# Optimization experiments

Hardware: AMD Instinct MI355X
Metric: run time of the kernel (lower is better)

Reference implementation:

```python
import jax, jax.numpy as jnp
import numpy as np

B, L, D, H, MLP = 8, 1024, 768, 12, 3072
DH = D // H
EPS = 1e-5


def setup_inputs() -> dict:
    key = jax.random.key(0)
    ks = jax.random.split(key, 8)
    s = 0.02
    return {
        "x": jax.random.normal(ks[0], (B, L, D), dtype=jnp.float32),
        "ln1_g": jnp.ones((D,), jnp.float32),
        "ln1_b": jnp.zeros((D,), jnp.float32),
        "w_qkv": jax.random.normal(ks[1], (3 * D, D), dtype=jnp.float32) * s,
        "w_out": jax.random.normal(ks[2], (D, D), dtype=jnp.float32) * s,
        "b_out": jnp.zeros((D,), jnp.float32),
        "ln2_g": jnp.ones((D,), jnp.float32),
        "ln2_b": jnp.zeros((D,), jnp.float32),
        "w1": jax.random.normal(ks[3], (MLP, D), dtype=jnp.float32) * s,
        "b1": jnp.zeros((MLP,), jnp.float32),
        "w2": jax.random.normal(ks[4], (D, MLP), dtype=jnp.float32) * s,
        "b2": jnp.zeros((D,), jnp.float32),
    }


def _layernorm(x, g, b):
    mu = jnp.mean(x, axis=-1, keepdims=True)
    var = jnp.mean(jnp.square(x - mu), axis=-1, keepdims=True)
    return (x - mu) * jax.lax.rsqrt(var + EPS) * g + b


def reference(x, ln1_g, ln1_b, w_qkv, w_out, b_out, ln2_g, ln2_b, w1, b1, w2, b2):
    # --- self-attention branch ---
    xn = _layernorm(x, ln1_g, ln1_b)                     # [B, L, D]
    qkv = jnp.einsum('bld,ed->ble', xn, w_qkv)           # [B, L, 3D]
    # rearrange 'b l (qkv h d) -> qkv b h l d'
    qkv = qkv.reshape(B, L, 3, H, DH).transpose(2, 0, 3, 1, 4)
    q, k, v = qkv[0], qkv[1], qkv[2]                     # [B, H, L, DH]
    scale = DH ** -0.5
    att = jnp.einsum('bhxd,bhyd->bhxy', q, k) * scale    # [B, H, L, L]
    att = jax.nn.softmax(att, axis=-1)
    o = jnp.einsum('bhxy,bhyd->bhxd', att, v)            # [B, H, L, DH]
    o = o.transpose(0, 2, 1, 3).reshape(B, L, D)         # 'b h l d -> b l (h d)'
    o = jnp.einsum('bld,ed->ble', o, w_out) + b_out
    x = x + o
    # --- MLP branch ---
    xn = _layernorm(x, ln2_g, ln2_b)
    h = jax.nn.gelu(jnp.einsum('bld,md->blm', xn, w1) + b1, approximate=False)
    h = jnp.einsum('blm,dm->bld', h, w2) + b2
    return x + h
```

## Files before the change

### kernel.cpp

```cpp
#include <hip/hip_runtime.h>
#include <hip/hip_bf16.h>
#include <math.h>

#define NB 8
#define NL 1024
#define ND 768
#define NH 12
#define NDH 64
#define NMLP 3072
#define NROWS 8192

typedef __attribute__((ext_vector_type(8))) short short8;
typedef __attribute__((ext_vector_type(8))) __bf16 bf16x8;
typedef __attribute__((ext_vector_type(4))) float f32x4;
typedef __attribute__((ext_vector_type(4))) float float4v;
typedef __attribute__((ext_vector_type(4))) unsigned short ushort4v;

__device__ __forceinline__ unsigned short f2b(float f) {
  unsigned u = __float_as_uint(f);
  unsigned r = (u + 0x7fffu + ((u >> 16) & 1u)) >> 16;
  return (unsigned short)r;
}

__device__ __forceinline__ f32x4 mfma16(short8 a, short8 b, f32x4 c) {
  return __builtin_amdgcn_mfma_f32_16x16x32_bf16(
      __builtin_bit_cast(bf16x8, a), __builtin_bit_cast(bf16x8, b), c, 0, 0, 0);
}

__device__ __forceinline__ void gl_lds16(const void* g, void* l) {
  __builtin_amdgcn_global_load_lds(
      (__attribute__((address_space(1))) void*)g,
      (__attribute__((address_space(3))) void*)l, 16, 0, 0);
}

__global__ __launch_bounds__(256) void cvt_all(const float* __restrict__ s0,
                                               const float* __restrict__ s1,
                                               const float* __restrict__ s2,
                                               const float* __restrict__ s3,
                                               unsigned short* __restrict__ d) {
  int i = (blockIdx.x * 256 + threadIdx.x) * 4;
  const float* s;
  int off;
  if (i < 1769472) { s = s0; off = i; }
  else if (i < 2359296) { s = s1; off = i - 1769472; }
  else if (i < 4718592) { s = s2; off = i - 2359296; }
  else { s = s3; off = i - 4718592; }
  float4v v = *(const float4v*)(s + off);
  ushort4v o;
  o[0] = f2b(v[0]); o[1] = f2b(v[1]); o[2] = f2b(v[2]); o[3] = f2b(v[3]);
  *(ushort4v*)(d + i) = o;
}

__global__ __launch_bounds__(256) void ln_bf16(const float* __restrict__ x,
                                               const float* __restrict__ g,
                                               const float* __restrict__ b,
                                               unsigned short* __restrict__ out) {
  int row = blockIdx.x, tid = threadIdx.x;
  const float* xr = x + (size_t)row * ND;
  float v0 = xr[tid], v1 = xr[tid + 256], v2 = xr[tid + 512];
  float s = v0 + v1 + v2;
  __shared__ float red[8];
#pragma unroll
  for (int o = 32; o > 0; o >>= 1) s += __shfl_down(s, o);
  int wv = tid >> 6, ln = tid & 63;
  if (ln == 0) red[wv] = s;
  __syncthreads();
  float mu = (red[0] + red[1] + red[2] + red[3]) * (1.0f / 768.0f);
  float d0 = v0 - mu, d1 = v1 - mu, d2 = v2 - mu;
  float q = d0 * d0 + d1 * d1 + d2 * d2;
#pragma unroll
  for (int o = 32; o > 0; o >>= 1) q += __shfl_down(q, o);
  if (ln == 0) red[4 + wv] = q;
  __syncthreads();
  float var = (red[4] + red[5] + red[6] + red[7]) * (1.0f / 768.0f);
  float rs = rsqrtf(var + 1e-5f);
  unsigned short* orow = out + (size_t)row * ND;
  orow[tid]       = f2b(d0 * rs * g[tid]       + b[tid]);
  orow[tid + 256] = f2b(d1 * rs * g[tid + 256] + b[tid + 256]);
  orow[tid + 512] = f2b(d2 * rs * g[tid + 512] + b[tid + 512]);
}

template <int MODE>
__global__ __launch_bounds__(512) void gemm128(
    const unsigned short* __restrict__ A, const unsigned short* __restrict__ W,
    unsigned short* __restrict__ outB, float* __restrict__ outF,
    const float* __restrict__ bias, const float* __restrict__ resid,
    int M, int N, int K, int gx) {
  __shared__ __attribute__((aligned(16))) unsigned short As[2 * 8192];
  __shared__ __attribute__((aligned(16))) unsigned short Bs[2 * 8192];

  const int nwg = gridDim.x;
  const int bid = blockIdx.x;
  const int q = nwg >> 3, r = nwg & 7;
  const int xcd = bid & 7, idx = bid >> 3;
  const int swz = (xcd < r ? xcd * (q + 1) : r * (q + 1) + (xcd - r) * q) + idx;
  const int by = swz / gx, bx = swz - by * gx;
  const int m0 = by * 128, n0 = bx * 128;

  const int tid = threadIdx.x;
  const int wave = tid >> 6, lane = tid & 63;
  const int l15 = lane & 15, lhi = lane >> 4;
  const int sw = l15 & 7;
  const int wm = wave >> 2, wn = wave & 3;

  const int sr = tid >> 3;
  const int swc8 = ((tid & 7) ^ (sr & 7)) * 8;
  const unsigned short* Aga = A + (size_t)(m0 + sr) * K + swc8;
  const unsigned short* Wga = W + (size_t)(n0 + sr) * K + swc8;

  f32x4 acc[4][2];
#pragma unroll
  for (int i = 0; i < 4; i++)
#pragma unroll
    for (int j = 0; j < 2; j++) acc[i][j] = (f32x4){0.f, 0.f, 0.f, 0.f};

  auto STAGE = [&](int kelem, int buf) {
    unsigned short* Ad = As + buf * 8192 + wave * 512;
    unsigned short* Bd = Bs + buf * 8192 + wave * 512;
    gl_lds16(Aga + kelem, Ad);
    gl_lds16(Aga + (size_t)64 * K + kelem, Ad + 4096);
    gl_lds16(Wga + kelem, Bd);
    gl_lds16(Wga + (size_t)64 * K + kelem, Bd + 4096);
  };

  const int NT = K >> 6;
  STAGE(0, 0);

  for (int t = 0; t < NT; ++t) {
    const int cb = t & 1;
    asm volatile("s_waitcnt vmcnt(0)" ::: "memory");
    __builtin_amdgcn_s_barrier();

    const unsigned short* Ac = As + cb * 8192;
    const unsigned short* Bc = Bs + cb * 8192;
    short8 af[4][2], bf[2][2];
#pragma unroll
    for (int i = 0; i < 4; i++) {
      int ar = wm * 64 + i * 16 + l15;
#pragma unroll
      for (int kk = 0; kk < 2; kk++)
        af[i][kk] = *(const short8*)&Ac[ar * 64 + (((kk * 4 + lhi) ^ sw) * 8)];
    }
#pragma unroll
    for (int j = 0; j < 2; j++) {
      int br = wn * 32 + j * 16 + l15;
#pragma unroll
      for (int kk = 0; kk < 2; kk++)
        bf[j][kk] = *(const short8*)&Bc[br * 64 + (((kk * 4 + lhi) ^ sw) * 8)];
    }
    if (t + 1 < NT) STAGE((t + 1) * 64, cb ^ 1);
#pragma unroll
    for (int kk = 0; kk < 2; kk++)
#pragma unroll
      for (int i = 0; i < 4; i++)
#pragma unroll
        for (int j = 0; j < 2; j++)
          acc[i][j] = mfma16(af[i][kk], bf[j][kk], acc[i][j]);
  }

#pragma unroll
  for (int i = 0; i < 4; i++) {
    int row = m0 + wm * 64 + i * 16 + lhi * 4;
#pragma unroll
    for (int j = 0; j < 2; j++) {
      int col = n0 + wn * 32 + j * 16 + l15;
#pragma unroll
      for (int r2 = 0; r2 < 4; r2++) {
        float v = acc[i][j][r2];
        size_t idxo = (size_t)(row + r2) * N + col;
        if (MODE == 0) {
          outB[idxo] = f2b(v);
        } else if (MODE == 2) {
          float t2 = v + bias[col];
          float z = 1.5957691f * t2 * (1.0f + 0.044715f * t2 * t2);
          float e = __expf(-z);
          outB[idxo] = f2b(__fdividef(t2, 1.0f + e));
        } else {
          outF[idxo] = v + bias[col] + resid[idxo];
        }
      }
    }
  }
}

template <int MODE>
__global__ __launch_bounds__(256) void gemm64(
    const unsigned short* __restrict__ A, const unsigned short* __restrict__ W,
    float* __restrict__ outF, const float* __restrict__ bias,
    const float* __restrict__ resid, int M, int N, int K, int gx) {
  __shared__ __attribute__((aligned(16))) unsigned short As[2 * 4096];
  __shared__ __attribute__((aligned(16))) unsigned short Bs[2 * 8192];

  const int nwg = gridDim.x;
  const int bid = blockIdx.x;
  const int q = nwg >> 3, r = nwg & 7;
  const int xcd = bid & 7, idx = bid >> 3;
  const int swz = (xcd < r ? xcd * (q + 1) : r * (q + 1) + (xcd - r) * q) + idx;
  const int by = swz / gx, bx = swz - by * gx;
  const int m0 = by * 64, n0 = bx * 128;

  const int tid = threadIdx.x;
  const int wave = tid >> 6, lane = tid & 63;
  const int l15 = lane & 15, lhi = lane >> 4;
  const int wn = wave;

  const int sr = tid >> 3;
  const int swc8 = ((tid & 7) ^ (sr & 7)) * 8;
  const unsigned short* Aga = A + (size_t)(m0 + sr) * K + swc8;
  const unsigned short* Wga = W + (size_t)(n0 + sr) * K + swc8;

  f32x4 acc[4][2];
#pragma unroll
  for (int i = 0; i < 4; i++)
#pragma unroll
    for (int j = 0; j < 2; j++) acc[i][j] = (f32x4){0.f, 0.f, 0.f, 0.f};

  auto STAGE = [&](int kelem, int buf) {
    unsigned short* Ad = As + buf * 4096 + wave * 512;
    unsigned short* Bd = Bs + buf * 8192 + wave * 512;
    gl_lds16(Aga + kelem, Ad);
    gl_lds16(Aga + (size_t)32 * K + kelem, Ad + 2048);
    gl_lds16(Wga + kelem, Bd);
    gl_lds16(Wga + (size_t)32 * K + kelem, Bd + 2048);
    gl_lds16(Wga + (size_t)64 * K + kelem, Bd + 4096);
    gl_lds16(Wga + (size_t)96 * K + kelem, Bd + 6144);
  };

  const int NT = K >> 6;
  STAGE(0, 0);

  for (int t = 0; t < NT; ++t) {
    const int cb = t & 1;
    if (t + 1 < NT) {
      STAGE((t + 1) * 64, cb ^ 1);
      asm volatile("s_waitcnt vmcnt(6)" ::: "memory");
    } else {
      asm volatile("s_waitcnt vmcnt(0)" ::: "memory");
    }
    __builtin_amdgcn_s_barrier();

    const unsigned short* Ac = As + cb * 4096;
    const unsigned short* Bc = Bs + cb * 8192;
    short8 af[4][2], bf[2][2];
#pragma unroll
    for (int i = 0; i < 4; i++) {
      int ar = i * 16 + l15;
#pragma unroll
      for (int kk = 0; kk < 2; kk++)
        af[i][kk] = *(const short8*)&Ac[ar * 64 + (((kk * 4 + lhi) ^ (ar & 7)) * 8)];
    }
#pragma unroll
    for (int j = 0; j < 2; j++) {
      int br = wn * 32 + j * 16 + l15;
#pragma unroll
      for (int kk = 0; kk < 2; kk++)
        bf[j][kk] = *(const short8*)&Bc[br * 64 + (((kk * 4 + lhi) ^ (br & 7)) * 8)];
    }
#pragma unroll
    for (int kk = 0; kk < 2; kk++)
#pragma unroll
      for (int i = 0; i < 4; i++)
#pragma unroll
        for (int j = 0; j < 2; j++)
          acc[i][j] = mfma16(af[i][kk], bf[j][kk], acc[i][j]);

    asm volatile("s_waitcnt lgkmcnt(0)" ::: "memory");
    __builtin_amdgcn_s_barrier();
  }

#pragma unroll
  for (int i = 0; i < 4; i++) {
    int row = m0 + i * 16 + lhi * 4;
#pragma unroll
    for (int j = 0; j < 2; j++) {
      int col = n0 + wn * 32 + j * 16 + l15;
#pragma unroll
      for (int r2 = 0; r2 < 4; r2++) {
        size_t idxo = (size_t)(row + r2) * N + col;
        outF[idxo] = acc[i][j][r2] + bias[col] + resid[idxo];
      }
    }
  }
}

__global__ __launch_bounds__(256) void vtrans(const unsigned short* __restrict__ qkv,
                                              unsigned short* __restrict__ vT) {
  int bid = blockIdx.x;
  int tt = bid & 15;
  int t2 = bid >> 4;
  int h = t2 % NH, b = t2 / NH;
  __shared__ unsigned short L[64 * 72];
  int t = threadIdx.x;
  int row0 = t >> 3;
  int col8 = (t & 7) * 8;
#pragma unroll
  for (int s = 0; s < 2; s++) {
    int row = row0 + s * 32;
    const unsigned short* src =
        qkv + ((size_t)(b * NL + tt * 64 + row)) * 2304 + 1536 + h * 64 + col8;
    short8 v = *(const short8*)src;
    int wchunk = row >> 3;
#pragma unroll
    for (int j = 0; j < 8; j++) {
      int d = col8 + j;
      int cp = wchunk ^ (d >> 3);
      L[d * 72 + cp * 8 + (row & 7)] = (unsigned short)v[j];
    }
  }
  __syncthreads();
#pragma unroll
  for (int s = 0; s < 2; s++) {
    int d = (t >> 3) + s * 32;
    int rc = t & 7;
    int cp = rc ^ (d >> 3);
    short8 ov = *(const short8*)&L[d * 72 + cp * 8];
    *(short8*)(vT + ((size_t)((b * NH + h) * 64 + d)) * NL + tt * 64 + rc * 8) = ov;
  }
}

#define L2E8 0.180336880f
__global__ __launch_bounds__(256, 3) void attn_kernel(
    const unsigned short* __restrict__ qkv, const unsigned short* __restrict__ vT,
    unsigned short* __restrict__ o) {
  int bid0 = blockIdx.x;
  int lb = (bid0 & 7) * 96 + (bid0 >> 3);
  int qt = lb & 7;
  int t = lb >> 3;
  int h = t % NH, b = t / NH;
  const int tid = threadIdx.x;
  const int wave = tid >> 6, lane = tid & 63;
  const int l15 = lane & 15, lhi = lane >> 4;
  const int sw = l15 & 7;
  __shared__ __attribute__((aligned(16))) unsigned short Ks[2 * 64 * 64];
  __shared__ __attribute__((aligned(16))) unsigned short Vs[2 * 64 * 64];
  __shared__ __attribute__((aligned(16))) unsigned short Ps[2 * 4 * 16 * 64];

  const unsigned short* qp = qkv + (size_t)(b * NL + qt * 128) * 2304 + h * 64;
  short8 qf[2][2];
#pragma unroll
  for (int i = 0; i < 2; i++)
#pragma unroll
    for (int kk = 0; kk < 2; kk++)
      qf[i][kk] = *(const short8*)(qp + (size_t)(i * 64 + wave * 16 + l15) * 2304 +
                                   kk * 32 + lhi * 8);

  const int srow = tid >> 3, scpos = tid & 7;
  const int sc8 = (scpos ^ (srow & 7)) * 8;
  const unsigned short* ks0 =
      qkv + (size_t)(b * NL + srow) * 2304 + 768 + h * 64 + sc8;
  const unsigned short* vt0 =
      vT + (size_t)((b * NH + h) * 64 + srow) * NL + sc8;
  unsigned short* Pw0 = Ps + wave * 1024;
  unsigned short* Pw1 = Ps + 4096 + wave * 1024;

  int paddr[4][4];
#pragma unroll
  for (int kb = 0; kb < 4; kb++) {
    int ch = kb * 2 + (l15 >> 3);
#pragma unroll
    for (int r = 0; r < 4; r++) {
      int row = lhi * 4 + r;
      paddr[kb][r] = row * 64 + ((ch ^ (row & 7)) << 3) + sw;
    }
  }

  f32x4 acc[2][4];
  f32x4 accL[2];
#pragma unroll
  for (int i = 0; i < 2; i++) {
    accL[i] = (f32x4){0.f, 0.f, 0.f, 0.f};
#pragma unroll
    for (int nb = 0; nb < 4; nb++) acc[i][nb] = (f32x4){0.f, 0.f, 0.f, 0.f};
  }

  short8 onesf;
#pragma unroll
  for (int j = 0; j < 8; j++) onesf[j] = (short)0x3F80;

#define STAGE(ktile, buf)                                                    \
  {                                                                          \
    const unsigned short* ksrc = ks0 + (size_t)((ktile) * 64) * 2304;        \
    const unsigned short* vsrc = vt0 + (ktile) * 64;                         \
    unsigned short* kb_ = Ks + (buf) * 4096 + wave * 512;                    \
    unsigned short* vb_ = Vs + (buf) * 4096 + wave * 512;                    \
    gl_lds16(ksrc, kb_);                                                     \
    gl_lds16(ksrc + (size_t)32 * 2304, kb_ + 2048);                          \
    gl_lds16(vsrc, vb_);                                                     \
    gl_lds16(vsrc + 32 * NL, vb_ + 2048);                                    \
  }

  STAGE(0, 0);

  for (int kt = 0; kt < 16; kt++) {
    const int cb = kt & 1;
    if (kt + 1 < 16) {
      STAGE(kt + 1, cb ^ 1);
      asm volatile("s_waitcnt vmcnt(4)" ::: "memory");
    } else {
      asm volatile("s_waitcnt vmcnt(0)" ::: "memory");
    }
    __builtin_amdgcn_s_barrier();

    const unsigned short* Kc = Ks + cb * 4096;
    const unsigned short* Vc = Vs + cb * 4096;

    f32x4 sv[2][4];
    __builtin_amdgcn_s_setprio(1);
#pragma unroll
    for (int kb = 0; kb < 4; kb++) {
      short8 kf0 = *(const short8*)&Kc[(kb * 16 + l15) * 64 + (lhi ^ sw) * 8];
      short8 kf1 = *(const short8*)&Kc[(kb * 16 + l15) * 64 + ((4 + lhi) ^ sw) * 8];
#pragma unroll
      for (int i = 0; i < 2; i++) {
        f32x4 s = mfma16(qf[i][0], kf0, (f32x4){0.f, 0.f, 0.f, 0.f});
        sv[i][kb] = mfma16(qf[i][1], kf1, s);
      }
    }
    __builtin_amdgcn_s_setprio(0);

    short8 vf[4][2];
#pragma unroll
    for (int nb = 0; nb < 4; nb++)
#pragma unroll
      for (int kk = 0; kk < 2; kk++)
        vf[nb][kk] =
            *(const short8*)&Vc[(nb * 16 + l15) * 64 + ((kk * 4 + lhi) ^ sw) * 8];

#pragma unroll
    for (int i = 0; i < 2; i++) {
      unsigned short* Pw = i ? Pw1 : Pw0;
#pragma unroll
      for (int kb = 0; kb < 4; kb++)
#pragma unroll
        for (int r = 0; r < 4; r++) {
          float p = exp2f(sv[i][kb][r] * L2E8);
          Pw[paddr[kb][r]] = (unsigned short)(__float_as_uint(p) >> 16);
        }
    }

    __builtin_amdgcn_s_setprio(1);
#pragma unroll
    for (int i = 0; i < 2; i++) {
      const unsigned short* Pw = i ? Pw1 : Pw0;
      short8 pf0 = *(const short8*)&Pw[l15 * 64 + (lhi ^ sw) * 8];
      short8 pf1 = *(const short8*)&Pw[l15 * 64 + ((4 + lhi) ^ sw) * 8];
#pragma unroll
      for (int nb = 0; nb < 4; nb++) {
        acc[i][nb] = mfma16(pf0, vf[nb][0], acc[i][nb]);
        acc[i][nb] = mfma16(pf1, vf[nb][1], acc[i][nb]);
      }
      accL[i] = mfma16(pf0, onesf, accL[i]);
      accL[i] = mfma16(pf1, onesf, accL[i]);
    }
    __builtin_amdgcn_s_setprio(0);
    __builtin_amdgcn_s_barrier();
  }
#undef STAGE

#pragma unroll
  for (int i = 0; i < 2; i++) {
    float inv[4];
#pragma unroll
    for (int r = 0; r < 4; r++) inv[r] = 1.0f / accL[i][r];
    size_t obase =
        (size_t)(b * NL + qt * 128 + i * 64 + wave * 16 + lhi * 4) * ND + h * 64;
#pragma unroll
    for (int nb = 0; nb < 4; nb++)
#pragma unroll
      for (int r = 0; r < 4; r++)
        o[obase + (size_t)r * ND + nb * 16 + l15] = f2b(acc[i][nb][r] * inv[r]);
  }
}

extern "C" void kernel_launch(void* const* d_in, const int* in_sizes, int n_in,
                              void* d_out, int out_size, void* d_ws, size_t ws_size,
                              hipStream_t stream) {
  const float* x     = (const float*)d_in[0];
  const float* ln1_g = (const float*)d_in[1];
  const float* ln1_b = (const float*)d_in[2];
  const float* w_qkv = (const float*)d_in[3];
  const float* w_out = (const float*)d_in[4];
  const float* b_out = (const float*)d_in[5];
  const float* ln2_g = (const float*)d_in[6];
  const float* ln2_b = (const float*)d_in[7];
  const float* w1    = (const float*)d_in[8];
  const float* b1    = (const float*)d_in[9];
  const float* w2    = (const float*)d_in[10];
  const float* b2    = (const float*)d_in[11];
  float* out = (float*)d_out;

  char* p = (char*)d_ws;
  unsigned short* wqkv_b = (unsigned short*)p; p += (size_t)2304 * 768 * 2;
  unsigned short* wout_b = (unsigned short*)p; p += (size_t)768 * 768 * 2;
  unsigned short* w1_b   = (unsigned short*)p; p += (size_t)3072 * 768 * 2;
  unsigned short* w2_b   = (unsigned short*)p; p += (size_t)768 * 3072 * 2;
  unsigned short* xn     = (unsigned short*)p; p += (size_t)NROWS * ND * 2;
  unsigned short* qkvb   = (unsigned short*)p; p += (size_t)NROWS * NMLP * 2;
  float* x1 = (float*)p;  p += (size_t)NROWS * ND * 4;
  unsigned short* vTb = (unsigned short*)x1;

  cvt_all<<<7077888 / 4 / 256, 256, 0, stream>>>(w_qkv, w_out, w1, w2, wqkv_b);

  ln_bf16<<<NROWS, 256, 0, stream>>>(x, ln1_g, ln1_b, xn);
  gemm128<0><<<1152, 512, 0, stream>>>(
      xn, wqkv_b, qkvb, nullptr, nullptr, nullptr, NROWS, 2304, 768, 18);
  vtrans<<<NB * NH * (NL / 64), 256, 0, stream>>>(qkvb, vTb);
  attn_kernel<<<NB * NH * (NL / 128), 256, 0, stream>>>(qkvb, vTb, xn);
  gemm64<1><<<768, 256, 0, stream>>>(
      xn, wout_b, x1, b_out, x, NROWS, 768, 768, 6);
  ln_bf16<<<NROWS, 256, 0, stream>>>(x1, ln2_g, ln2_b, xn);
  gemm128<2><<<1536, 512, 0, stream>>>(
      xn, w1_b, qkvb, nullptr, b1, nullptr, NROWS, 3072, 768, 24);
  gemm128<3><<<384, 512, 0, stream>>>(
      qkvb, w2_b, nullptr, out, b2, x1, NROWS, 768, 3072, 6);
}
```

Measured before the change: 250.6 us.

## Make gemm128 blocks loop over several N tiles, shrinking grids

Each gemm128 workgroup now computes nbx consecutive 128-wide N tiles in sequence rather than one. The grid shrinks to match (QKV 1152→384, MLP1 1536→512). The first K-slice of the next tile is prefetched during the last iteration of the current one, so the double buffer keeps running across tiles. This is meant to cut launch and wave-scheduling overhead and the per-workgroup prologue, with tiles that share an A block kept in one workgroup. The cost is fewer workgroups in flight on the 256-CU device, so the tail and parallelism may suffer. A tiles are still reloaded for each N tile.

```diff
diff --git a/kernel.cpp b/kernel.cpp
--- a/kernel.cpp
+++ b/kernel.cpp
@@ -85,7 +85,7 @@
     const unsigned short* __restrict__ A, const unsigned short* __restrict__ W,
     unsigned short* __restrict__ outB, float* __restrict__ outF,
     const float* __restrict__ bias, const float* __restrict__ resid,
-    int M, int N, int K, int gx) {
+    int M, int N, int K, int gx, int nbx) {
   __shared__ __attribute__((aligned(16))) unsigned short As[2 * 8192];
   __shared__ __attribute__((aligned(16))) unsigned short Bs[2 * 8192];
 
@@ -94,8 +94,8 @@
   const int q = nwg >> 3, r = nwg & 7;
   const int xcd = bid & 7, idx = bid >> 3;
   const int swz = (xcd < r ? xcd * (q + 1) : r * (q + 1) + (xcd - r) * q) + idx;
-  const int by = swz / gx, bx = swz - by * gx;
-  const int m0 = by * 128, n0 = bx * 128;
+  const int by = swz / gx, bxg = swz - by * gx;
+  const int m0 = by * 128;
 
   const int tid = threadIdx.x;
   const int wave = tid >> 6, lane = tid & 63;
@@ -106,15 +106,9 @@
   const int sr = tid >> 3;
   const int swc8 = ((tid & 7) ^ (sr & 7)) * 8;
   const unsigned short* Aga = A + (size_t)(m0 + sr) * K + swc8;
-  const unsigned short* Wga = W + (size_t)(n0 + sr) * K + swc8;
-
-  f32x4 acc[4][2];
-#pragma unroll
-  for (int i = 0; i < 4; i++)
-#pragma unroll
-    for (int j = 0; j < 2; j++) acc[i][j] = (f32x4){0.f, 0.f, 0.f, 0.f};
-
-  auto STAGE = [&](int kelem, int buf) {
+  const unsigned short* WgaB = W + (size_t)sr * K + swc8;
+
+  auto STAGE = [&](const unsigned short* Wga, int kelem, int buf) {
     unsigned short* Ad = As + buf * 8192 + wave * 512;
     unsigned short* Bd = Bs + buf * 8192 + wave * 512;
     gl_lds16(Aga + kelem, Ad);
@@ -124,59 +118,76 @@
   };
 
   const int NT = K >> 6;
-  STAGE(0, 0);
-
-  for (int t = 0; t < NT; ++t) {
-    const int cb = t & 1;
-    asm volatile("s_waitcnt vmcnt(0)" ::: "memory");
-    __builtin_amdgcn_s_barrier();
-
-    const unsigned short* Ac = As + cb * 8192;
-    const unsigned short* Bc = Bs + cb * 8192;
-    short8 af[4][2], bf[2][2];
+  {
+    const unsigned short* Wga0 = WgaB + (size_t)(bxg * nbx) * 128 * K;
+    STAGE(Wga0, 0, 0);
+  }
+
+  for (int bxt = 0; bxt < nbx; ++bxt) {
+    const int bx = bxg * nbx + bxt;
+    const int n0 = bx * 128;
+    const unsigned short* Wga = WgaB + (size_t)bx * 128 * K;
+    const unsigned short* WgaN = WgaB + (size_t)(bx + 1) * 128 * K;
+
+    f32x4 acc[4][2];
+#pragma unroll
+    for (int i = 0; i < 4; i++)
+#pragma unroll
+      for (int j = 0; j < 2; j++) acc[i][j] = (f32x4){0.f, 0.f, 0.f, 0.f};
+
+    for (int t = 0; t < NT; ++t) {
+      const int cb = t & 1;
+      asm volatile("s_waitcnt vmcnt(0)" ::: "memory");
+      __builtin_amdgcn_s_barrier();
+
+      const unsigned short* Ac = As + cb * 8192;
+      const unsigned short* Bc = Bs + cb * 8192;
+      short8 af[4][2], bf[2][2];
+#pragma unroll
+      for (int i = 0; i < 4; i++) {
+        int ar = wm * 64 + i * 16 + l15;
+#pragma unroll
+        for (int kk = 0; kk < 2; kk++)
+          af[i][kk] = *(const short8*)&Ac[ar * 64 + (((kk * 4 + lhi) ^ sw) * 8)];
+      }
+#pragma unroll
+      for (int j = 0; j < 2; j++) {
+        int br = wn * 32 + j * 16 + l15;
+#pragma unroll
+        for (int kk = 0; kk < 2; kk++)
+          bf[j][kk] = *(const short8*)&Bc[br * 64 + (((kk * 4 + lhi) ^ sw) * 8)];
+      }
+      if (t + 1 < NT) STAGE(Wga, (t + 1) * 64, cb ^ 1);
+      else if (bxt + 1 < nbx) STAGE(WgaN, 0, cb ^ 1);
+#pragma unroll
+      for (int kk = 0; kk < 2; kk++)
+#pragma unroll
+        for (int i = 0; i < 4; i++)
+#pragma unroll
+          for (int j = 0; j < 2; j++)
+            acc[i][j] = mfma16(af[i][kk], bf[j][kk], acc[i][j]);
+    }
+
 #pragma unroll
     for (int i = 0; i < 4; i++) {
-      int ar = wm * 64 + i * 16 + l15;
-#pragma unroll
-      for (int kk = 0; kk < 2; kk++)
-        af[i][kk] = *(const short8*)&Ac[ar * 64 + (((kk * 4 + lhi) ^ sw) * 8)];
-    }
-#pragma unroll
-    for (int j = 0; j < 2; j++) {
-      int br = wn * 32 + j * 16 + l15;
-#pragma unroll
-      for (int kk = 0; kk < 2; kk++)
-        bf[j][kk] = *(const short8*)&Bc[br * 64 + (((kk * 4 + lhi) ^ sw) * 8)];
-    }
-    if (t + 1 < NT) STAGE((t + 1) * 64, cb ^ 1);
-#pragma unroll
-    for (int kk = 0; kk < 2; kk++)
-#pragma unroll
-      for (int i = 0; i < 4; i++)
-#pragma unroll
-        for (int j = 0; j < 2; j++)
-          acc[i][j] = mfma16(af[i][kk], bf[j][kk], acc[i][j]);
-  }
-
-#pragma unroll
-  for (int i = 0; i < 4; i++) {
-    int row = m0 + wm * 64 + i * 16 + lhi * 4;
-#pragma unroll
-    for (int j = 0; j < 2; j++) {
-      int col = n0 + wn * 32 + j * 16 + l15;
-#pragma unroll
-      for (int r2 = 0; r2 < 4; r2++) {
-        float v = acc[i][j][r2];
-        size_t idxo = (size_t)(row + r2) * N + col;
-        if (MODE == 0) {
-          outB[idxo] = f2b(v);
-        } else if (MODE == 2) {
-          float t2 = v + bias[col];
-          float z = 1.5957691f * t2 * (1.0f + 0.044715f * t2 * t2);
-          float e = __expf(-z);
-          outB[idxo] = f2b(__fdividef(t2, 1.0f + e));
-        } else {
-          outF[idxo] = v + bias[col] + resid[idxo];
+      int row = m0 + wm * 64 + i * 16 + lhi * 4;
+#pragma unroll
+      for (int j = 0; j < 2; j++) {
+        int col = n0 + wn * 32 + j * 16 + l15;
+#pragma unroll
+        for (int r2 = 0; r2 < 4; r2++) {
+          float v = acc[i][j][r2];
+          size_t idxo = (size_t)(row + r2) * N + col;
+          if (MODE == 0) {
+            outB[idxo] = f2b(v);
+          } else if (MODE == 2) {
+            float t2 = v + bias[col];
+            float z = 1.5957691f * t2 * (1.0f + 0.044715f * t2 * t2);
+            float e = __expf(-z);
+            outB[idxo] = f2b(__fdividef(t2, 1.0f + e));
+          } else {
+            outF[idxo] = v + bias[col] + resid[idxo];
+          }
         }
       }
     }
@@ -502,15 +513,15 @@
   cvt_all<<<7077888 / 4 / 256, 256, 0, stream>>>(w_qkv, w_out, w1, w2, wqkv_b);
 
   ln_bf16<<<NROWS, 256, 0, stream>>>(x, ln1_g, ln1_b, xn);
-  gemm128<0><<<1152, 512, 0, stream>>>(
-      xn, wqkv_b, qkvb, nullptr, nullptr, nullptr, NROWS, 2304, 768, 18);
+  gemm128<0><<<384, 512, 0, stream>>>(
+      xn, wqkv_b, qkvb, nullptr, nullptr, nullptr, NROWS, 2304, 768, 6, 3);
   vtrans<<<NB * NH * (NL / 64), 256, 0, stream>>>(qkvb, vTb);
   attn_kernel<<<NB * NH * (NL / 128), 256, 0, stream>>>(qkvb, vTb, xn);
   gemm64<1><<<768, 256, 0, stream>>>(
       xn, wout_b, x1, b_out, x, NROWS, 768, 768, 6);
   ln_bf16<<<NROWS, 256, 0, stream>>>(x1, ln2_g, ln2_b, xn);
-  gemm128<2><<<1536, 512, 0, stream>>>(
-      xn, w1_b, qkvb, nullptr, b1, nullptr, NROWS, 3072, 768, 24);
+  gemm128<2><<<512, 512, 0, stream>>>(
+      xn, w1_b, qkvb, nullptr, b1, nullptr, NROWS, 3072, 768, 8, 3);
   gemm128<3><<<384, 512, 0, stream>>>(
-      qkvb, w2_b, nullptr, out, b2, x1, NROWS, 768, 3072, 6);
-}
+      qkvb, w2_b, nullptr, out, b2, x1, NROWS, 768, 3072, 6, 1);
+}
```

New measurement: 297.4 us. 18.7% more time.
